# Kernel tuning notes

Hardware: AMD Instinct MI355X
Metric: run time of the kernel (lower is better)

Reference implementation:

```python
import math
import jax, jax.numpy as jnp
import numpy as np

B, T, H = 2, 2048, 1024
NH, WINDOW = 16, 256
HD = H // NH


def setup_inputs() -> dict:
    key = jax.random.key(0)
    ks = jax.random.split(key, 4)
    x = jax.random.normal(ks[0], (B, T, H), dtype=jnp.float32)
    # init scales match nn.Linear default fan-in uniform roughly; exact init irrelevant for correctness
    W_qkv = jax.random.normal(ks[1], (H, 3 * H), dtype=jnp.float32) * (1.0 / math.sqrt(H))
    b_qkv = jnp.zeros((3 * H,), dtype=jnp.float32)
    W_out = jax.random.normal(ks[2], (H, H), dtype=jnp.float32) * (1.0 / math.sqrt(H))
    b_out = jnp.zeros((H,), dtype=jnp.float32)
    return {"x": x, "W_qkv": W_qkv, "b_qkv": b_qkv, "W_out": W_out, "b_out": b_out}


def reference(x, W_qkv, b_qkv, W_out, b_out):
    b, t, h = x.shape
    qkv = x @ W_qkv + b_qkv                      # [B, T, 3H]
    qkv = qkv.reshape(b, t, 3, NH, HD)           # (three nh hd) split order
    qkv = jnp.transpose(qkv, (2, 0, 3, 1, 4))    # [3, B, nh, T, hd]
    q, k, v = qkv[0], qkv[1], qkv[2]
    scores = jnp.einsum('bnid,bnjd->bnij', q, k) / math.sqrt(HD)  # [B, nh, T, T]
    idx = jnp.arange(t)
    diff = idx[:, None] - idx[None, :]           # i - j
    mask = (diff < 0) | (diff >= WINDOW)         # causal + window band
    scores = jnp.where(mask[None, None], -jnp.inf, scores)
    attn = jax.nn.softmax(scores, axis=-1)
    out = jnp.einsum('bnij,bnjd->bnid', attn, v)  # [B, nh, T, hd]
    out = jnp.transpose(out, (0, 2, 1, 3)).reshape(b, t, h)
    return out @ W_out + b_out
```

## Files before the change

kernel.cpp:

```cpp
#include <hip/hip_runtime.h>

typedef unsigned short u16;
typedef __attribute__((ext_vector_type(8))) __bf16 bf16x8;
typedef __attribute__((ext_vector_type(4))) float f32x4;
typedef __attribute__((ext_vector_type(8))) u16 u16x8;

#define MFMA(a, b, c) __builtin_amdgcn_mfma_f32_16x16x32_bf16((a), (b), (c), 0, 0, 0)

#define TT 2048
#define NHEAD 16
#define HDIM 64

__device__ __forceinline__ u16 f2bf(float f) {
  union { float f; unsigned u; } v; v.f = f;
  unsigned r = (v.u + 0x7fffu + ((v.u >> 16) & 1u)) >> 16;
  return (u16)r;
}

__device__ __forceinline__ void gll16(const u16* g, u16* l) {
  __builtin_amdgcn_global_load_lds(
      (__attribute__((address_space(1))) void*)g,
      (__attribute__((address_space(3))) void*)l, 16, 0, 0);
}

__global__ __launch_bounds__(256) void cvt_bf16_k(const float* __restrict__ in,
                                                  u16* __restrict__ out) {
  int i = blockIdx.x * 256 + threadIdx.x;
  float4 a = ((const float4*)in)[2 * i];
  float4 b = ((const float4*)in)[2 * i + 1];
  u16x8 r;
  r[0] = f2bf(a.x); r[1] = f2bf(a.y); r[2] = f2bf(a.z); r[3] = f2bf(a.w);
  r[4] = f2bf(b.x); r[5] = f2bf(b.y); r[6] = f2bf(b.z); r[7] = f2bf(b.w);
  ((u16x8*)out)[i] = r;
}

__global__ __launch_bounds__(256) void transpose_cvt_k(const float* __restrict__ in,
                                                       u16* __restrict__ out,
                                                       int R, int C) {
  __shared__ float tile[32][33];
  int tx = threadIdx.x & 31, ty = threadIdx.x >> 5;
  int r0 = blockIdx.y * 32, c0 = blockIdx.x * 32;
#pragma unroll
  for (int i = 0; i < 4; ++i)
    tile[ty + i * 8][tx] = in[(size_t)(r0 + ty + i * 8) * C + c0 + tx];
  __syncthreads();
#pragma unroll
  for (int i = 0; i < 4; ++i)
    out[(size_t)(c0 + ty + i * 8) * R + r0 + tx] = f2bf(tile[tx][ty + i * 8]);
}

__device__ __forceinline__ void gemm_core(const u16* __restrict__ A,
                                          const u16* __restrict__ Bt,
                                          int m0, int n0,
                                          u16* As, u16* Bs, f32x4 acc[4][4]) {
  const int tid = threadIdx.x;
  const int w = tid >> 6, lane = tid & 63;
  const int wr = w >> 1, wc = w & 1;
  const int lr = lane & 15, lk = (lane >> 4) << 3;
  const int srow = w << 5;
  const u16* ga = A + (size_t)(m0 + srow + (lane >> 2)) * 1024 + ((lane & 3) << 3);
  const u16* gb = Bt + (size_t)(n0 + srow + (lane >> 2)) * 1024 + ((lane & 3) << 3);
  u16* la = As + srow * 32;
  u16* lb = Bs + srow * 32;
  for (int k0 = 0; k0 < 1024; k0 += 32) {
#pragma unroll
    for (int i = 0; i < 2; ++i) {
      gll16(ga + i * 16384 + k0, la + i * 512);
      gll16(gb + i * 16384 + k0, lb + i * 512);
    }
    __syncthreads();
    bf16x8 af[4], bfr[4];
#pragma unroll
    for (int m = 0; m < 4; ++m)
      af[m] = *(const bf16x8*)(As + ((wr << 6) + m * 16 + lr) * 32 + lk);
#pragma unroll
    for (int n = 0; n < 4; ++n)
      bfr[n] = *(const bf16x8*)(Bs + ((wc << 6) + n * 16 + lr) * 32 + lk);
#pragma unroll
    for (int m = 0; m < 4; ++m)
#pragma unroll
      for (int n = 0; n < 4; ++n)
        acc[m][n] = MFMA(af[m], bfr[n], acc[m][n]);
    __syncthreads();
  }
}

__global__ __launch_bounds__(256) void gemm_qkv_k(const u16* __restrict__ A,
                                                  const u16* __restrict__ Bt,
                                                  const float* __restrict__ bias,
                                                  u16* __restrict__ qo,
                                                  u16* __restrict__ ko,
                                                  u16* __restrict__ vto) {
  __shared__ __align__(16) u16 As[128 * 32];
  __shared__ __align__(16) u16 Bs[128 * 32];
  f32x4 acc[4][4] = {};
  const int m0 = blockIdx.y << 7, n0 = blockIdx.x << 7;
  gemm_core(A, Bt, m0, n0, As, Bs, acc);
  const int tid = threadIdx.x, w = tid >> 6, lane = tid & 63;
  const int wr = w >> 1, wc = w & 1, lr = lane & 15, lg = lane >> 4;
  const int gcb = n0 + (wc << 6);
  const int three = gcb >> 10;
  const int nh = (gcb & 1023) >> 6;
#pragma unroll
  for (int n = 0; n < 4; ++n) {
    const int hd = n * 16 + lr;
    const float bv = bias[gcb + hd];
#pragma unroll
    for (int m = 0; m < 4; ++m) {
#pragma unroll
      for (int r = 0; r < 4; ++r) {
        const int grow = m0 + (wr << 6) + m * 16 + (lg << 2) + r;
        const int bb = grow >> 11, t = grow & 2047;
        const float val = acc[m][n][r] + bv;
        const int head = (bb << 4) + nh;
        if (three == 0)
          qo[((size_t)head * TT + t) * HDIM + hd] = f2bf(val * 0.125f);
        else if (three == 1)
          ko[((size_t)head * TT + t) * HDIM + hd] = f2bf(val);
        else
          vto[((size_t)head * HDIM + hd) * TT + t] = f2bf(val);
      }
    }
  }
}

__global__ __launch_bounds__(256) void attn_win_k(const u16* __restrict__ Q,
                                                  const u16* __restrict__ K,
                                                  const u16* __restrict__ Vt,
                                                  u16* __restrict__ O) {
  __shared__ __align__(16) u16 Pl[4][16][40];
  const int tid = threadIdx.x, w = tid >> 6, lane = tid & 63;
  const int head = blockIdx.y;
  const int t0w = blockIdx.x * 64 + w * 16;
  const u16* Qh = Q + (size_t)head * TT * HDIM;
  const u16* Kh = K + (size_t)head * TT * HDIM;
  const u16* Vh = Vt + (size_t)head * HDIM * TT;
  const int lr = lane & 15, lg = lane >> 4;

  bf16x8 qa0 = *(const bf16x8*)(Qh + (size_t)(t0w + lr) * HDIM + lg * 8);
  bf16x8 qa1 = *(const bf16x8*)(Qh + (size_t)(t0w + lr) * HDIM + 32 + lg * 8);

  f32x4 o0 = {}, o1 = {}, o2 = {}, o3 = {};
  float m[4], lsum[4];
#pragma unroll
  for (int r = 0; r < 4; ++r) { m[r] = -1e30f; lsum[r] = 0.f; }

  const int jstart = (t0w > 255) ? ((t0w - 255) & ~31) : 0;
  const int jlast = t0w + 15;
  for (int j0 = jstart; j0 <= jlast; j0 += 32) {
    f32x4 s[2];
#pragma unroll
    for (int n = 0; n < 2; ++n) {
      const u16* kp = Kh + (size_t)(j0 + n * 16 + lr) * HDIM + lg * 8;
      f32x4 z = {};
      z = MFMA(qa0, *(const bf16x8*)kp, z);
      z = MFMA(qa1, *(const bf16x8*)(kp + 32), z);
      s[n] = z;
    }
    const int row0 = t0w + (lg << 2);
    float tm[4];
#pragma unroll
    for (int r = 0; r < 4; ++r) {
      const int i = row0 + r;
#pragma unroll
      for (int n = 0; n < 2; ++n) {
        const int j = j0 + n * 16 + lr;
        const bool valid = (j <= i) && (i - j < 256);
        s[n][r] = valid ? s[n][r] : -1e30f;
      }
      tm[r] = fmaxf(s[0][r], s[1][r]);
    }
#pragma unroll
    for (int d = 1; d < 16; d <<= 1)
#pragma unroll
      for (int r = 0; r < 4; ++r) tm[r] = fmaxf(tm[r], __shfl_xor(tm[r], d));
    float sc[4], rs[4];
#pragma unroll
    for (int r = 0; r < 4; ++r) {
      const float mn = fmaxf(m[r], tm[r]);
      sc[r] = __expf(m[r] - mn);
      m[r] = mn;
      rs[r] = 0.f;
    }
#pragma unroll
    for (int n = 0; n < 2; ++n)
#pragma unroll
      for (int r = 0; r < 4; ++r) {
        const float p = __expf(s[n][r] - m[r]);
        s[n][r] = p;
        rs[r] += p;
      }
#pragma unroll
    for (int d = 1; d < 16; d <<= 1)
#pragma unroll
      for (int r = 0; r < 4; ++r) rs[r] += __shfl_xor(rs[r], d);
#pragma unroll
    for (int r = 0; r < 4; ++r) {
      lsum[r] = lsum[r] * sc[r] + rs[r];
      o0[r] *= sc[r]; o1[r] *= sc[r]; o2[r] *= sc[r]; o3[r] *= sc[r];
    }
#pragma unroll
    for (int n = 0; n < 2; ++n)
#pragma unroll
      for (int r = 0; r < 4; ++r)
        Pl[w][(lg << 2) + r][n * 16 + lr] = f2bf(s[n][r]);
    asm volatile("s_waitcnt lgkmcnt(0)" ::: "memory");
    bf16x8 pa = *(const bf16x8*)&Pl[w][lr][lg * 8];
    const u16* vp = Vh + (size_t)lr * TT + j0 + lg * 8;
    o0 = MFMA(pa, *(const bf16x8*)(vp), o0);
    o1 = MFMA(pa, *(const bf16x8*)(vp + 16 * TT), o1);
    o2 = MFMA(pa, *(const bf16x8*)(vp + 32 * TT), o2);
    o3 = MFMA(pa, *(const bf16x8*)(vp + 48 * TT), o3);
  }
  const int bb = head >> 4, nh = head & 15;
#pragma unroll
  for (int r = 0; r < 4; ++r) {
    const float inv = 1.0f / lsum[r];
    const int i = t0w + (lg << 2) + r;
    u16* op = O + ((size_t)bb * TT + i) * 1024 + nh * 64 + lr;
    op[0]  = f2bf(o0[r] * inv);
    op[16] = f2bf(o1[r] * inv);
    op[32] = f2bf(o2[r] * inv);
    op[48] = f2bf(o3[r] * inv);
  }
}

__global__ __launch_bounds__(256) void gemm_out_k(const u16* __restrict__ A,
                                                  const u16* __restrict__ Bt,
                                                  const float* __restrict__ bias,
                                                  float* __restrict__ out) {
  __shared__ __align__(16) u16 As[128 * 32];
  __shared__ __align__(16) u16 Bs[128 * 32];
  f32x4 acc[4][4] = {};
  const int m0 = blockIdx.y << 7, n0 = blockIdx.x << 7;
  gemm_core(A, Bt, m0, n0, As, Bs, acc);
  const int tid = threadIdx.x, w = tid >> 6, lane = tid & 63;
  const int wr = w >> 1, wc = w & 1, lr = lane & 15, lg = lane >> 4;
#pragma unroll
  for (int n = 0; n < 4; ++n) {
    const int gc = n0 + (wc << 6) + n * 16 + lr;
    const float bv = bias[gc];
#pragma unroll
    for (int m = 0; m < 4; ++m)
#pragma unroll
      for (int r = 0; r < 4; ++r) {
        const int grow = m0 + (wr << 6) + m * 16 + (lg << 2) + r;
        out[(size_t)grow * 1024 + gc] = acc[m][n][r] + bv;
      }
  }
}

extern "C" void kernel_launch(void* const* d_in, const int* in_sizes, int n_in,
                              void* d_out, int out_size, void* d_ws, size_t ws_size,
                              hipStream_t stream) {
  (void)in_sizes; (void)n_in; (void)out_size; (void)ws_size;
  const float* x    = (const float*)d_in[0];
  const float* Wqkv = (const float*)d_in[1];
  const float* bqkv = (const float*)d_in[2];
  const float* Wout = (const float*)d_in[3];
  const float* bout = (const float*)d_in[4];
  float* out = (float*)d_out;

  u16* ws    = (u16*)d_ws;
  u16* xb    = ws;
  u16* wqkvT = xb + 4194304;
  u16* woutT = wqkvT + 3145728;
  u16* qb    = woutT + 1048576;
  u16* kb    = qb + 4194304;
  u16* vtb   = kb + 4194304;
  u16* aob   = vtb + 4194304;

  cvt_bf16_k<<<2048, 256, 0, stream>>>(x, xb);
  transpose_cvt_k<<<dim3(3072 / 32, 1024 / 32), 256, 0, stream>>>(Wqkv, wqkvT, 1024, 3072);
  transpose_cvt_k<<<dim3(1024 / 32, 1024 / 32), 256, 0, stream>>>(Wout, woutT, 1024, 1024);
  gemm_qkv_k<<<dim3(24, 32), 256, 0, stream>>>(xb, wqkvT, bqkv, qb, kb, vtb);
  attn_win_k<<<dim3(32, 32), 256, 0, stream>>>(qb, kb, vtb, aob);
  gemm_out_k<<<dim3(8, 32), 256, 0, stream>>>(aob, woutT, bout, out);
}
```

Measured before the change: 187.8 us.

## Widen attention key tile, compute row sums via MFMA, shrink out-proj GEMM tile

The attention kernel now handles 64 keys per iteration instead of 32, and it computes the softmax denominator with an MFMA against a vector of ones instead of shuffle reductions. This halves the loop trip count and drops one cross-lane reduction per iteration, but it does more masked work at the window edges. Separately, the output projection GEMM uses a 64x128 tile with its own simple k-loop, which doubles the block count to 512 to improve occupancy across CUs. That loop has no double buffering.

```diff
diff --git a/kernel.cpp b/kernel.cpp
--- a/kernel.cpp
+++ b/kernel.cpp
@@ -128,7 +128,7 @@
                                                   const u16* __restrict__ K,
                                                   const u16* __restrict__ Vt,
                                                   u16* __restrict__ O) {
-  __shared__ __align__(16) u16 Pl[4][16][40];
+  __shared__ __align__(16) u16 Pl[4][16][72];
   const int tid = threadIdx.x, w = tid >> 6, lane = tid & 63;
   const int head = blockIdx.y;
   const int t0w = blockIdx.x * 64 + w * 16;
@@ -140,17 +140,22 @@
   bf16x8 qa0 = *(const bf16x8*)(Qh + (size_t)(t0w + lr) * HDIM + lg * 8);
   bf16x8 qa1 = *(const bf16x8*)(Qh + (size_t)(t0w + lr) * HDIM + 32 + lg * 8);
 
-  f32x4 o0 = {}, o1 = {}, o2 = {}, o3 = {};
-  float m[4], lsum[4];
-#pragma unroll
-  for (int r = 0; r < 4; ++r) { m[r] = -1e30f; lsum[r] = 0.f; }
-
-  const int jstart = (t0w > 255) ? ((t0w - 255) & ~31) : 0;
+  union { u16x8 u; bf16x8 b; } uo;
+#pragma unroll
+  for (int i = 0; i < 8; ++i) uo.u[i] = 0x3F80;
+  const bf16x8 ones = uo.b;
+
+  f32x4 o0 = {}, o1 = {}, o2 = {}, o3 = {}, osum = {};
+  float m[4];
+#pragma unroll
+  for (int r = 0; r < 4; ++r) m[r] = -1e30f;
+
+  const int jstart = (t0w > 255) ? ((t0w - 255) & ~63) : 0;
   const int jlast = t0w + 15;
-  for (int j0 = jstart; j0 <= jlast; j0 += 32) {
-    f32x4 s[2];
-#pragma unroll
-    for (int n = 0; n < 2; ++n) {
+  for (int j0 = jstart; j0 <= jlast; j0 += 64) {
+    f32x4 s[4];
+#pragma unroll
+    for (int n = 0; n < 4; ++n) {
       const u16* kp = Kh + (size_t)(j0 + n * 16 + lr) * HDIM + lg * 8;
       f32x4 z = {};
       z = MFMA(qa0, *(const bf16x8*)kp, z);
@@ -163,59 +168,58 @@
     for (int r = 0; r < 4; ++r) {
       const int i = row0 + r;
 #pragma unroll
-      for (int n = 0; n < 2; ++n) {
+      for (int n = 0; n < 4; ++n) {
         const int j = j0 + n * 16 + lr;
         const bool valid = (j <= i) && (i - j < 256);
         s[n][r] = valid ? s[n][r] : -1e30f;
       }
-      tm[r] = fmaxf(s[0][r], s[1][r]);
+      tm[r] = fmaxf(fmaxf(s[0][r], s[1][r]), fmaxf(s[2][r], s[3][r]));
     }
 #pragma unroll
     for (int d = 1; d < 16; d <<= 1)
 #pragma unroll
       for (int r = 0; r < 4; ++r) tm[r] = fmaxf(tm[r], __shfl_xor(tm[r], d));
-    float sc[4], rs[4];
+    float sc[4];
 #pragma unroll
     for (int r = 0; r < 4; ++r) {
       const float mn = fmaxf(m[r], tm[r]);
       sc[r] = __expf(m[r] - mn);
       m[r] = mn;
-      rs[r] = 0.f;
-    }
-#pragma unroll
-    for (int n = 0; n < 2; ++n)
-#pragma unroll
-      for (int r = 0; r < 4; ++r) {
-        const float p = __expf(s[n][r] - m[r]);
-        s[n][r] = p;
-        rs[r] += p;
-      }
-#pragma unroll
-    for (int d = 1; d < 16; d <<= 1)
-#pragma unroll
-      for (int r = 0; r < 4; ++r) rs[r] += __shfl_xor(rs[r], d);
+    }
+#pragma unroll
+    for (int n = 0; n < 4; ++n)
+#pragma unroll
+      for (int r = 0; r < 4; ++r)
+        s[n][r] = __expf(s[n][r] - m[r]);
 #pragma unroll
     for (int r = 0; r < 4; ++r) {
-      lsum[r] = lsum[r] * sc[r] + rs[r];
       o0[r] *= sc[r]; o1[r] *= sc[r]; o2[r] *= sc[r]; o3[r] *= sc[r];
-    }
-#pragma unroll
-    for (int n = 0; n < 2; ++n)
+      osum[r] *= sc[r];
+    }
+#pragma unroll
+    for (int n = 0; n < 4; ++n)
 #pragma unroll
       for (int r = 0; r < 4; ++r)
         Pl[w][(lg << 2) + r][n * 16 + lr] = f2bf(s[n][r]);
     asm volatile("s_waitcnt lgkmcnt(0)" ::: "memory");
-    bf16x8 pa = *(const bf16x8*)&Pl[w][lr][lg * 8];
+    bf16x8 pa0 = *(const bf16x8*)&Pl[w][lr][lg * 8];
+    bf16x8 pa1 = *(const bf16x8*)&Pl[w][lr][32 + lg * 8];
     const u16* vp = Vh + (size_t)lr * TT + j0 + lg * 8;
-    o0 = MFMA(pa, *(const bf16x8*)(vp), o0);
-    o1 = MFMA(pa, *(const bf16x8*)(vp + 16 * TT), o1);
-    o2 = MFMA(pa, *(const bf16x8*)(vp + 32 * TT), o2);
-    o3 = MFMA(pa, *(const bf16x8*)(vp + 48 * TT), o3);
+    o0 = MFMA(pa0, *(const bf16x8*)(vp), o0);
+    o0 = MFMA(pa1, *(const bf16x8*)(vp + 32), o0);
+    o1 = MFMA(pa0, *(const bf16x8*)(vp + 16 * TT), o1);
+    o1 = MFMA(pa1, *(const bf16x8*)(vp + 16 * TT + 32), o1);
+    o2 = MFMA(pa0, *(const bf16x8*)(vp + 32 * TT), o2);
+    o2 = MFMA(pa1, *(const bf16x8*)(vp + 32 * TT + 32), o2);
+    o3 = MFMA(pa0, *(const bf16x8*)(vp + 48 * TT), o3);
+    o3 = MFMA(pa1, *(const bf16x8*)(vp + 48 * TT + 32), o3);
+    osum = MFMA(pa0, ones, osum);
+    osum = MFMA(pa1, ones, osum);
   }
   const int bb = head >> 4, nh = head & 15;
 #pragma unroll
   for (int r = 0; r < 4; ++r) {
-    const float inv = 1.0f / lsum[r];
+    const float inv = 1.0f / osum[r];
     const int i = t0w + (lg << 2) + r;
     u16* op = O + ((size_t)bb * TT + i) * 1024 + nh * 64 + lr;
     op[0]  = f2bf(o0[r] * inv);
@@ -229,22 +233,45 @@
                                                   const u16* __restrict__ Bt,
                                                   const float* __restrict__ bias,
                                                   float* __restrict__ out) {
-  __shared__ __align__(16) u16 As[128 * 32];
+  __shared__ __align__(16) u16 As[64 * 32];
   __shared__ __align__(16) u16 Bs[128 * 32];
-  f32x4 acc[4][4] = {};
-  const int m0 = blockIdx.y << 7, n0 = blockIdx.x << 7;
-  gemm_core(A, Bt, m0, n0, As, Bs, acc);
+  f32x4 acc[2][4] = {};
+  const int m0 = blockIdx.y << 6, n0 = blockIdx.x << 7;
   const int tid = threadIdx.x, w = tid >> 6, lane = tid & 63;
   const int wr = w >> 1, wc = w & 1, lr = lane & 15, lg = lane >> 4;
+  const int lk = lg << 3;
+  const u16* ga = A + (size_t)(m0 + (w << 4) + (lane >> 2)) * 1024 + ((lane & 3) << 3);
+  const u16* gb = Bt + (size_t)(n0 + (w << 5) + (lane >> 2)) * 1024 + ((lane & 3) << 3);
+  u16* la = As + (w << 4) * 32;
+  u16* lb = Bs + (w << 5) * 32;
+  for (int k0 = 0; k0 < 1024; k0 += 32) {
+    gll16(ga + k0, la);
+    gll16(gb + k0, lb);
+    gll16(gb + 16384 + k0, lb + 512);
+    __syncthreads();
+    bf16x8 af[2], bfr[4];
+#pragma unroll
+    for (int m = 0; m < 2; ++m)
+      af[m] = *(const bf16x8*)(As + ((wr << 5) + m * 16 + lr) * 32 + lk);
+#pragma unroll
+    for (int n = 0; n < 4; ++n)
+      bfr[n] = *(const bf16x8*)(Bs + ((wc << 6) + n * 16 + lr) * 32 + lk);
+#pragma unroll
+    for (int m = 0; m < 2; ++m)
+#pragma unroll
+      for (int n = 0; n < 4; ++n)
+        acc[m][n] = MFMA(af[m], bfr[n], acc[m][n]);
+    __syncthreads();
+  }
 #pragma unroll
   for (int n = 0; n < 4; ++n) {
     const int gc = n0 + (wc << 6) + n * 16 + lr;
     const float bv = bias[gc];
 #pragma unroll
-    for (int m = 0; m < 4; ++m)
+    for (int m = 0; m < 2; ++m)
 #pragma unroll
       for (int r = 0; r < 4; ++r) {
-        const int grow = m0 + (wr << 6) + m * 16 + (lg << 2) + r;
+        const int grow = m0 + (wr << 5) + m * 16 + (lg << 2) + r;
         out[(size_t)grow * 1024 + gc] = acc[m][n][r] + bv;
       }
   }
@@ -275,5 +302,5 @@
   transpose_cvt_k<<<dim3(1024 / 32, 1024 / 32), 256, 0, stream>>>(Wout, woutT, 1024, 1024);
   gemm_qkv_k<<<dim3(24, 32), 256, 0, stream>>>(xb, wqkvT, bqkv, qb, kb, vtb);
   attn_win_k<<<dim3(32, 32), 256, 0, stream>>>(qb, kb, vtb, aob);
-  gemm_out_k<<<dim3(8, 32), 256, 0, stream>>>(aob, woutT, bout, out);
-}
+  gemm_out_k<<<dim3(8, 64), 256, 0, stream>>>(aob, woutT, bout, out);
+}
```

Result: no change. 188.3 us (+0.3%).
